# Kernel tuning notes

Measured on AMD Instinct MI355X. Metric: run time of the kernel, lower is better.

## Reference

```python
import jax, jax.numpy as jnp
import numpy as np

# dims: C=d_model, DI=expand*C (d_inner), S=d_state, R=dt_rank, K=4 scan dirs
C, DI, S, R, K = 64, 128, 16, 4, 4
Hh, Ww, T, Bsz = 48, 48, 4, 1

def _silu(x):
    return x * jax.nn.sigmoid(x)

def _ln_c(x, w, b, eps=1e-6):
    # LayerNorm2d: normalize over channel dim of [B,C,H,W]
    mu = jnp.mean(x, axis=1, keepdims=True)
    var = jnp.var(x, axis=1, keepdims=True)
    return (x - mu) * jax.lax.rsqrt(var + eps) * w[None, :, None, None] + b[None, :, None, None]

def _cal_kl(cur, prev):
    # elementwise KL over channel-softmax distributions, shape-preserving
    lp = jax.nn.log_softmax(prev, axis=1)
    lq = jax.nn.log_softmax(cur, axis=1)
    return jnp.exp(lp) * (lp - lq)

def _ss2d(x, in_w, in_b, cw, cb, xp_w, dt_w, dt_b, A_logs, Ds, onw, onb, ow, ob):
    # VMamba-style SS2D, channel-first input [B,C,H,W]
    B_, _, H_, W_ = x.shape
    L = H_ * W_
    xz = jnp.einsum('dc,bchw->bdhw', in_w, x) + in_b[None, :, None, None]
    xc, z = jnp.split(xz, 2, axis=1)
    di = xc.shape[1]
    xc = jax.lax.conv_general_dilated(xc, cw[:, None], (1, 1), 'SAME',
        dimension_numbers=('NCHW', 'OIHW', 'NCHW'), feature_group_count=di)
    xc = _silu(xc + cb[None, :, None, None])
    # cross-scan: row-major, col-major, and their reverses -> [B,K,DI,L]
    x1 = xc.reshape(B_, di, L)
    x2 = jnp.swapaxes(xc, 2, 3).reshape(B_, di, L)
    xs = jnp.stack([x1, x2, jnp.flip(x1, -1), jnp.flip(x2, -1)], axis=1)
    xdbl = jnp.einsum('krd,bkdl->bkrl', xp_w, xs)
    dts, Bs, Cs = jnp.split(xdbl, [R, R + S], axis=2)  # [B,K,R,L],[B,K,S,L],[B,K,S,L]
    dt = jax.nn.softplus(jnp.einsum('kdr,bkrl->bkdl', dt_w, dts) + dt_b[None, :, :, None])
    A = -jnp.exp(A_logs)  # [K,DI,S]
    dA = jnp.exp(dt[..., None] * A[None, :, :, None, :])                    # [B,K,DI,L,S]
    dBx = (dt * xs)[..., None] * jnp.swapaxes(Bs, 2, 3)[:, :, None, :, :]   # [B,K,DI,L,S]
    def comb(e1, e2):
        a1, b1 = e1
        a2, b2 = e2
        return (a1 * a2, a2 * b1 + b2)
    _, hs = jax.lax.associative_scan(comb, (dA, dBx), axis=3)
    y = jnp.einsum('bkdls,bksl->bkdl', hs, Cs) + Ds[None, :, :, None] * xs
    # cross-merge back to row-major and sum
    y0 = y[:, 0]
    y1 = jnp.swapaxes(y[:, 1].reshape(B_, di, W_, H_), 2, 3).reshape(B_, di, L)
    y2 = jnp.flip(y[:, 2], -1)
    y3 = jnp.swapaxes(jnp.flip(y[:, 3], -1).reshape(B_, di, W_, H_), 2, 3).reshape(B_, di, L)
    yy = (y0 + y1 + y2 + y3).reshape(B_, di, H_, W_)
    yy = _ln_c(yy, onw, onb) * _silu(z)
    return jnp.einsum('cd,bdhw->bchw', ow, yy) + ob[None, :, None, None]

def setup_inputs():
    key = jax.random.key(0)
    ks = jax.random.split(key, 16)
    rn = lambda k, shp, s: jax.random.normal(k, shp, jnp.float32) * s
    return {
        'image_sequence': rn(ks[0], (Bsz, T, C, Hh, Ww), 1.0),
        'difficult_zone': rn(ks[1], (Bsz, C, Hh, Ww), 1.0),
        'sigma': rn(ks[2], (Bsz, C, Hh, Ww), 0.1),
        # params stacked over the 2 SS2D modules: [0]=mamba_sigma, [1]=mamba_bias
        'in_w': rn(ks[3], (2, 2 * DI, C), C ** -0.5),
        'in_b': rn(ks[4], (2, 2 * DI), 0.02),
        'conv_w': rn(ks[5], (2, DI, 3, 3), 1.0 / 3.0),
        'conv_b': rn(ks[6], (2, DI), 0.02),
        'xp_w': rn(ks[7], (2, K, R + 2 * S, DI), DI ** -0.5),
        'dt_w': rn(ks[8], (2, K, DI, R), R ** -0.5),
        'dt_b': rn(ks[9], (2, K, DI), 0.5),
        'A_logs': jnp.log(1.0 + jax.random.uniform(ks[10], (2, K, DI, S), jnp.float32)),
        'Ds': rn(ks[11], (2, K, DI), 0.5),
        'onw': jnp.ones((2, DI), jnp.float32),
        'onb': jnp.zeros((2, DI), jnp.float32),
        'ow': rn(ks[12], (2, C, DI), 0.02),
        'ob': jnp.zeros((2, C), jnp.float32),
        'niw': jnp.ones((C,), jnp.float32),
        'nib': jnp.zeros((C,), jnp.float32),
        'ndw': jnp.ones((C,), jnp.float32),
        'ndb': jnp.zeros((C,), jnp.float32),
    }

def reference(image_sequence, difficult_zone, sigma, in_w, in_b, conv_w, conv_b, xp_w, dt_w, dt_b, A_logs, Ds, onw, onb, ow, ob, niw, nib, ndw, ndb):
    prev = _ln_c(difficult_zone, ndw, ndb)
    cur = prev * jnp.exp(sigma)  # prev / exp(-sigma)
    for t in range(T):  # strictly sequential recurrence over `length` steps
        s = _ss2d(_cal_kl(cur, prev), in_w[0], in_b[0], conv_w[0], conv_b[0], xp_w[0],
                  dt_w[0], dt_b[0], A_logs[0], Ds[0], onw[0], onb[0], ow[0], ob[0])
        bias = _ss2d(_ln_c(image_sequence[:, t], niw, nib), in_w[1], in_b[1], conv_w[1], conv_b[1], xp_w[1],
                     dt_w[1], dt_b[1], A_logs[1], Ds[1], onw[1], onb[1], ow[1], ob[1])
        cur, prev = cur * jnp.exp(s) + bias, cur
    return cur
```

## Files before the change

kernel.cpp:

```cpp
#include <hip/hip_runtime.h>

#define DEV __device__ __forceinline__

constexpr int Cc = 64, DIc = 128, Sc = 16, Rc = 4, Kc = 4;
constexpr int Lc = 2304, Tc = 4;
constexpr int NCH = 144, CHL = 16;

constexpr int OFF_XCPRE = 0;
constexpr int OFF_Z     = 294912;
constexpr int OFF_XACT  = 589824;
constexpr int OFF_DTS   = 884736;
constexpr int OFF_BS    = 921600;
constexpr int OFF_CS    = 1069056;
constexpr int OFF_Y     = 1216512;
constexpr int OFF_SUMA  = 2396160;
constexpr int OFF_SUMB  = 3575808;
constexpr int OFF_H0    = 4755456;
constexpr int SLOTF     = 5935104;
constexpr int OFF_B1    = 5 * SLOTF;
constexpr int OFF_B2    = OFF_B1 + Lc * Cc;
constexpr int OFF_BIAS  = OFF_B2 + Lc * Cc;
constexpr int OFF_TW    = OFF_BIAS + Tc * Lc * Cc;
constexpr int TW_INW  = 0;
constexpr int TW_XPW  = 32768;
constexpr int TW_OW   = 69632;
constexpr int TW_CW   = 86016;
constexpr int TW_AT   = 88320;
constexpr int TW_DTW  = 104704;

struct Params {
  const float *img, *dz, *sigma, *in_w, *in_b, *conv_w, *conv_b, *xp_w, *dt_w,
              *dt_b, *A_logs, *Ds, *onw, *onb, *ow, *ob, *niw, *nib, *ndw, *ndb;
  float* outp;
  float* ws;
};

DEV float wsum(float v) {
#pragma unroll
  for (int m = 32; m; m >>= 1) v += __shfl_xor(v, m, 64);
  return v;
}
DEV float wmax(float v) {
#pragma unroll
  for (int m = 32; m; m >>= 1) v = fmaxf(v, __shfl_xor(v, m, 64));
  return v;
}
DEV float sigmoidf(float x) { return 1.f / (1.f + __expf(-x)); }
DEV float softplusf(float v) { return (v > 20.f) ? v : __logf(1.f + __expf(v)); }
DEV float fexp2(float x) { return __builtin_amdgcn_exp2f(x); }

DEV int perm_idx(int k, int l) {
  if (k == 0) return l;
  if (k == 1) return (l % 48) * 48 + l / 48;
  if (k == 2) return Lc - 1 - l;
  int pp = Lc - 1 - l;
  return (pp % 48) * 48 + pp / 48;
}

DEV int perm_stride(int k) {
  return (k == 0) ? 1 : (k == 1) ? 48 : (k == 2) ? -1 : -48;
}

__global__ __launch_bounds__(256) void g_transpose(Params p) {
  float* tw = p.ws + OFF_TW;
  int i = blockIdx.x * 256 + threadIdx.x;
  if (i < 32768) {
    int d = i & 255, cc = (i >> 8) & 63, b = i >> 14;
    tw[TW_INW + i] = p.in_w[(b * 256 + d) * 64 + cc];
  }
  if (i < 36864) {
    int kr = i % 144, cc = (i / 144) & 127, b = i / (144 * 128);
    tw[TW_XPW + i] = p.xp_w[(b * 144 + kr) * 128 + cc];
  }
  if (i < 16384) {
    int c = i & 63, d = (i >> 6) & 127, b = i >> 13;
    tw[TW_OW + i] = p.ow[(b * 64 + c) * 128 + d];
  }
  if (i < 2304) {
    int d = i & 127, kk = (i >> 7) % 9, b = i / 1152;
    tw[TW_CW + i] = p.conv_w[(b * 128 + d) * 9 + kk];
  }
  if (i < 16384) {
    int d = i & 127, bks = i >> 7;
    int s = bks & 15, bk = bks >> 4;
    tw[TW_AT + i] = -__expf(p.A_logs[(bk * 128 + d) * 16 + s]) * 1.4426950408889634f;
  }
  if (i < 4096) {
    int d = i & 127, bkr = i >> 7;
    int r = bkr & 3, bk = bkr >> 2;
    tw[TW_DTW + i] = p.dt_w[(bk * 128 + d) * 4 + r];
  }
}

__global__ __launch_bounds__(256) void g_inproj(Params p) {
  __shared__ float xv[8][64];
  int tid = threadIdx.x;
  int slot = blockIdx.y;
  int branch = (slot >= 4) ? 0 : 1;
  float* ws = p.ws;
  float* base = ws + (size_t)slot * SLOTF;
  float* xcpre = base + OFF_XCPRE;
  float* zbuf  = base + OFF_Z;
  const float* wT = ws + OFF_TW + TW_INW + branch * 64 * 256;
  int l0 = blockIdx.x * 8;
  int wv = tid >> 6, c = tid & 63;
#pragma unroll
  for (int q = 0; q < 2; q++) {
    int pp = wv * 2 + q;
    int l = l0 + pp;
    float x;
    if (branch == 1) {
      float v = p.img[(slot * Cc + c) * Lc + l];
      float mu = wsum(v) * (1.f / 64.f);
      float var = wsum(v * v) * (1.f / 64.f) - mu * mu;
      x = (v - mu) * rsqrtf(var + 1e-6f) * p.niw[c] + p.nib[c];
    } else {
      float v = p.dz[c * Lc + l];
      float mu = wsum(v) * (1.f / 64.f);
      float var = wsum(v * v) * (1.f / 64.f) - mu * mu;
      float pv = (v - mu) * rsqrtf(var + 1e-6f) * p.ndw[c] + p.ndb[c];
      float cv = pv * __expf(p.sigma[c * Lc + l]);
      (ws + OFF_B1)[l * Cc + c] = cv;
      float mp = wmax(pv);
      float sp = wsum(__expf(pv - mp));
      float lp = pv - mp - __logf(sp);
      float mq = wmax(cv);
      float sq = wsum(__expf(cv - mq));
      float lq = cv - mq - __logf(sq);
      x = __expf(lp) * (lp - lq);
    }
    xv[pp][c] = x;
  }
  __syncthreads();
  int d = tid;
  float acc[8];
#pragma unroll
  for (int q = 0; q < 8; q++) acc[q] = 0.f;
  for (int cc = 0; cc < Cc; cc++) {
    float wval = wT[cc * 256 + d];
#pragma unroll
    for (int q = 0; q < 8; q++) acc[q] += wval * xv[q][cc];
  }
  float bv = p.in_b[branch * 2 * DIc + d];
  if (d < DIc) {
#pragma unroll
    for (int q = 0; q < 8; q++) xcpre[(l0 + q) * DIc + d] = acc[q] + bv;
  } else {
    int dd = d - DIc;
#pragma unroll
    for (int q = 0; q < 8; q++) zbuf[(l0 + q) * DIc + dd] = acc[q] + bv;
  }
}

__global__ __launch_bounds__(256) void g_conv(Params p, int slot_base) {
  __shared__ float xv[4][DIc];
  int tid = threadIdx.x;
  int slot = slot_base + blockIdx.y;
  int branch = (slot >= 4) ? 0 : 1;
  float* ws = p.ws;
  float* base = ws + (size_t)slot * SLOTF;
  float* xcpre = base + OFF_XCPRE;
  float* xact  = base + OFF_XACT;
  float* dtsb  = base + OFF_DTS;
  float* Bsb   = base + OFF_BS;
  float* Csb   = base + OFF_CS;
  const float* cwT  = ws + OFF_TW + TW_CW + branch * 9 * 128;
  const float* xpwT = ws + OFF_TW + TW_XPW + branch * 128 * 144;
  int h = blockIdx.x / 12;
  int w0 = (blockIdx.x % 12) * 4;
  for (int it = tid; it < 4 * DIc; it += 256) {
    int d = it & (DIc - 1);
    int pp = it >> 7;
    int w = w0 + pp;
    float acc = 0.f;
#pragma unroll
    for (int kh = 0; kh < 3; kh++) {
      int hh = h + kh - 1;
      if ((unsigned)hh < 48u) {
#pragma unroll
        for (int kw = 0; kw < 3; kw++) {
          int wp = w + kw - 1;
          if ((unsigned)wp < 48u)
            acc += cwT[(kh * 3 + kw) * 128 + d] * xcpre[(hh * 48 + wp) * DIc + d];
        }
      }
    }
    float v = acc + p.conv_b[branch * DIc + d];
    float s = v * sigmoidf(v);
    xv[pp][d] = s;
    xact[(h * 48 + w) * DIc + d] = s;
  }
  __syncthreads();
  if (tid < Kc * 36) {
    int k = tid / 36, r = tid % 36;
    float acc[4] = {0.f, 0.f, 0.f, 0.f};
    for (int cc = 0; cc < DIc; cc++) {
      float wvv = xpwT[cc * 144 + tid];
#pragma unroll
      for (int pp = 0; pp < 4; pp++) acc[pp] += wvv * xv[pp][cc];
    }
#pragma unroll
    for (int pp = 0; pp < 4; pp++) {
      int w = w0 + pp;
      int lr = h * 48 + w, lcx = w * 48 + h;
      int pos = (k == 0) ? lr : (k == 1) ? lcx : (k == 2) ? (Lc - 1 - lr) : (Lc - 1 - lcx);
      if (r < Rc) dtsb[(k * Lc + pos) * Rc + r] = acc[pp];
      else if (r < Rc + Sc) Bsb[(k * Lc + pos) * Sc + (r - Rc)] = acc[pp];
      else Csb[(k * Lc + pos) * Sc + (r - Rc - Sc)] = acc[pp];
    }
  }
}

__global__ __launch_bounds__(256, 4) void g_scan1(Params p, int slot_base) {
  __shared__ alignas(16) float2 sDt[CHL][DIc];
  __shared__ alignas(16) float sB[CHL * Sc];
  __shared__ float sCT[2][DIc];
  int tid = threadIdx.x;
  int slot = slot_base + blockIdx.y;
  int branch = (slot >= 4) ? 0 : 1;
  float* ws = p.ws;
  float* base = ws + (size_t)slot * SLOTF;
  const float* xact = base + OFF_XACT;
  const float* Bsb  = base + OFF_BS;
  const float* dtsb = base + OFF_DTS;
  float* sumA = base + OFF_SUMA;
  float* sumB = base + OFF_SUMB;
  int bx = blockIdx.x;
  int k = bx / NCH, ch = bx - k * NCH;
  int d = tid & (DIc - 1);
  int sh = tid >> 7;
  int bk = branch * Kc + k;
  const float* AT   = ws + OFF_TW + TW_AT;
  const float* dtwT = ws + OFF_TW + TW_DTW;
  int l0 = ch * CHL;
  sB[tid] = Bsb[(k * Lc + l0) * Sc + tid];
  float A2[8];
#pragma unroll
  for (int j = 0; j < 8; j++) A2[j] = AT[(bk * 16 + sh * 8 + j) * 128 + d];
  int idx0 = perm_idx(k, l0);
  int st = perm_stride(k);
  float xw[8];
#pragma unroll
  for (int j = 0; j < 8; j++) xw[j] = xact[(idx0 + st * (sh * 8 + j)) * DIc + d];
  float4 dtq[8];
#pragma unroll
  for (int j = 0; j < 8; j++)
    dtq[j] = *(const float4*)(dtsb + (size_t)(k * Lc + l0 + sh * 8 + j) * 4);
  float dw0 = dtwT[(bk * 4 + 0) * 128 + d];
  float dw1 = dtwT[(bk * 4 + 1) * 128 + d];
  float dw2 = dtwT[(bk * 4 + 2) * 128 + d];
  float dw3 = dtwT[(bk * 4 + 3) * 128 + d];
  float db = p.dt_b[bk * DIc + d];
  float ct = 0.f;
#pragma unroll
  for (int j = 0; j < 8; j++) {
    float v = db + dw0 * dtq[j].x + dw1 * dtq[j].y + dw2 * dtq[j].z + dw3 * dtq[j].w;
    float dtv = softplusf(v);
    sDt[sh * 8 + j][d] = make_float2(dtv, dtv * xw[j]);
    ct += dtv;
  }
  sCT[sh][d] = ct;
  __syncthreads();
  float CT = sCT[0][d] + sCT[1][d];
  const float4* B4 = (const float4*)sB;
  float h0 = 0.f, h1 = 0.f, h2 = 0.f, h3 = 0.f, h4 = 0.f, h5 = 0.f, h6 = 0.f, h7 = 0.f;
#pragma unroll
  for (int ib = 0; ib < 4; ib++) {
    float2 dg[4];
    float4 Bg0[4], Bg1[4];
#pragma unroll
    for (int q = 0; q < 4; q++) {
      int i = ib * 4 + q;
      dg[q]  = sDt[i][d];
      Bg0[q] = B4[i * 4 + sh * 2];
      Bg1[q] = B4[i * 4 + sh * 2 + 1];
    }
#pragma unroll
    for (int q = 0; q < 4; q++) {
      float dtv = dg[q].x, dtx = dg[q].y;
#define STEP1(hh, bb, aa2) { float da = fexp2(dtv * (aa2)); hh = da * hh + dtx * (bb); }
      STEP1(h0, Bg0[q].x, A2[0]);
      STEP1(h1, Bg0[q].y, A2[1]);
      STEP1(h2, Bg0[q].z, A2[2]);
      STEP1(h3, Bg0[q].w, A2[3]);
      STEP1(h4, Bg1[q].x, A2[4]);
      STEP1(h5, Bg1[q].y, A2[5]);
      STEP1(h6, Bg1[q].z, A2[6]);
      STEP1(h7, Bg1[q].w, A2[7]);
#undef STEP1
    }
  }
  float* sa = sumA + ((size_t)(k * NCH + ch) * Sc + sh * 8) * DIc + d;
  float* sb = sumB + ((size_t)(k * NCH + ch) * Sc + sh * 8) * DIc + d;
#pragma unroll
  for (int j = 0; j < 8; j++) sa[j * DIc] = fexp2(A2[j] * CT);
  sb[0 * DIc] = h0; sb[1 * DIc] = h1; sb[2 * DIc] = h2; sb[3 * DIc] = h3;
  sb[4 * DIc] = h4; sb[5 * DIc] = h5; sb[6 * DIc] = h6; sb[7 * DIc] = h7;
}

__global__ __launch_bounds__(256) void g_mid(Params p, int slot_base) {
  int gid = blockIdx.x * 256 + threadIdx.x;
  int slot = slot_base + blockIdx.y;
  float* base = p.ws + (size_t)slot * SLOTF;
  const float* sumA = base + OFF_SUMA;
  const float* sumB = base + OFF_SUMB;
  float* h0 = base + OFF_H0;
  int d = gid & (DIc - 1);
  int s = (gid >> 7) & (Sc - 1);
  int k = gid >> 11;
  float h = 0.f;
  for (int g = 0; g < NCH / 16; g++) {
    float a[16], b[16];
#pragma unroll
    for (int j = 0; j < 16; j++) {
      int idx = ((k * NCH + g * 16 + j) * Sc + s) * DIc + d;
      a[j] = sumA[idx];
      b[j] = sumB[idx];
    }
#pragma unroll
    for (int j = 0; j < 16; j++) {
      int idx = ((k * NCH + g * 16 + j) * Sc + s) * DIc + d;
      h0[idx] = h;
      h = a[j] * h + b[j];
    }
  }
}

__global__ __launch_bounds__(256, 4) void g_scan2(Params p, int slot_base) {
  __shared__ alignas(16) float2 sDt[CHL][DIc];
  __shared__ alignas(16) float sB[CHL * Sc];
  __shared__ alignas(16) float sC[CHL * Sc];
  int tid = threadIdx.x;
  int slot = slot_base + blockIdx.y;
  int branch = (slot >= 4) ? 0 : 1;
  float* ws = p.ws;
  float* base = ws + (size_t)slot * SLOTF;
  const float* xact = base + OFF_XACT;
  const float* Bsb  = base + OFF_BS;
  const float* Csb  = base + OFF_CS;
  const float* dtsb = base + OFF_DTS;
  const float* h0b  = base + OFF_H0;
  float* yb = base + OFF_Y;
  int bx = blockIdx.x;
  int k = bx / NCH, ch = bx - k * NCH;
  int d = tid & (DIc - 1);
  int sh = tid >> 7;
  int bk = branch * Kc + k;
  const float* AT   = ws + OFF_TW + TW_AT;
  const float* dtwT = ws + OFF_TW + TW_DTW;
  int l0 = ch * CHL;
  sB[tid] = Bsb[(k * Lc + l0) * Sc + tid];
  sC[tid] = Csb[(k * Lc + l0) * Sc + tid];
  float A2[8];
#pragma unroll
  for (int j = 0; j < 8; j++) A2[j] = AT[(bk * 16 + sh * 8 + j) * 128 + d];
  float hr0, hr1, hr2, hr3, hr4, hr5, hr6, hr7;
  {
    const float* hp = h0b + ((size_t)(k * NCH + ch) * Sc + sh * 8) * DIc + d;
    hr0 = hp[0 * DIc]; hr1 = hp[1 * DIc]; hr2 = hp[2 * DIc]; hr3 = hp[3 * DIc];
    hr4 = hp[4 * DIc]; hr5 = hp[5 * DIc]; hr6 = hp[6 * DIc]; hr7 = hp[7 * DIc];
  }
  int idx0 = perm_idx(k, l0);
  int st = perm_stride(k);
  float xw[8];
#pragma unroll
  for (int j = 0; j < 8; j++) xw[j] = xact[(idx0 + st * (sh * 8 + j)) * DIc + d];
  float4 dtq[8];
#pragma unroll
  for (int j = 0; j < 8; j++)
    dtq[j] = *(const float4*)(dtsb + (size_t)(k * Lc + l0 + sh * 8 + j) * 4);
  float dw0 = dtwT[(bk * 4 + 0) * 128 + d];
  float dw1 = dtwT[(bk * 4 + 1) * 128 + d];
  float dw2 = dtwT[(bk * 4 + 2) * 128 + d];
  float dw3 = dtwT[(bk * 4 + 3) * 128 + d];
  float db = p.dt_b[bk * DIc + d];
  float Dv = p.Ds[bk * DIc + d];
#pragma unroll
  for (int j = 0; j < 8; j++) {
    float v = db + dw0 * dtq[j].x + dw1 * dtq[j].y + dw2 * dtq[j].z + dw3 * dtq[j].w;
    float dtv = softplusf(v);
    sDt[sh * 8 + j][d] = make_float2(dtv, dtv * xw[j]);
  }
  __syncthreads();
  const float4* B4 = (const float4*)sB;
  const float4* C4 = (const float4*)sC;
  float acc[CHL];
#pragma unroll
  for (int ib = 0; ib < 4; ib++) {
    float2 dg[4];
    float4 Bg0[4], Bg1[4];
#pragma unroll
    for (int q = 0; q < 4; q++) {
      int i = ib * 4 + q;
      dg[q]  = sDt[i][d];
      Bg0[q] = B4[i * 4 + sh * 2];
      Bg1[q] = B4[i * 4 + sh * 2 + 1];
    }
#pragma unroll
    for (int q = 0; q < 4; q++) {
      int i = ib * 4 + q;
      float4 Cg0 = C4[i * 4 + sh * 2];
      float4 Cg1 = C4[i * 4 + sh * 2 + 1];
      float dtv = dg[q].x, dtx = dg[q].y;
      float a = 0.f;
#define STEP(hh, bb, cc, aa2) { float da = fexp2(dtv * (aa2)); hh = da * hh + dtx * (bb); a += hh * (cc); }
      STEP(hr0, Bg0[q].x, Cg0.x, A2[0]);
      STEP(hr1, Bg0[q].y, Cg0.y, A2[1]);
      STEP(hr2, Bg0[q].z, Cg0.z, A2[2]);
      STEP(hr3, Bg0[q].w, Cg0.w, A2[3]);
      STEP(hr4, Bg1[q].x, Cg1.x, A2[4]);
      STEP(hr5, Bg1[q].y, Cg1.y, A2[5]);
      STEP(hr6, Bg1[q].z, Cg1.z, A2[6]);
      STEP(hr7, Bg1[q].w, Cg1.w, A2[7]);
#undef STEP
      acc[i] = a;
    }
  }
  if (sh == 0) {
#pragma unroll
    for (int j = 0; j < 8; j++) acc[j] += Dv * xw[j];
  } else {
#pragma unroll
    for (int j = 0; j < 8; j++) acc[8 + j] += Dv * xw[j];
  }
  __syncthreads();
  float* yred = (float*)sDt;
  if (sh == 1) {
#pragma unroll
    for (int i = 0; i < CHL; i++) yred[i * DIc + d] = acc[i];
  }
  __syncthreads();
  if (sh == 0) {
#pragma unroll
    for (int i = 0; i < CHL; i++)
      yb[(size_t)(k * Lc + l0 + i) * DIc + d] = acc[i] + yred[i * DIc + d];
  }
}

__global__ __launch_bounds__(256) void g_out_bias(Params p) {
  __shared__ float yy[4][DIc];
  __shared__ float ml[4][DIc];
  __shared__ float mnv[4], isv[4];
  int tid = threadIdx.x;
  int slot = blockIdx.y;
  float* ws = p.ws;
  float* base = ws + (size_t)slot * SLOTF;
  const float* yb = base + OFF_Y;
  const float* zb = base + OFF_Z;
  const float* owT = ws + OFF_TW + TW_OW + 128 * 64;
  float* biasb = ws + OFF_BIAS;
  int l0 = blockIdx.x * 4;
  for (int it = tid; it < 4 * DIc; it += 256) {
    int d = it & (DIc - 1), pp = it >> 7;
    int l = l0 + pp;
    int www = l % 48, hh = l / 48;
    int lr = l, lcx = www * 48 + hh;
    float v = yb[(0 * Lc + lr) * DIc + d] + yb[(1 * Lc + lcx) * DIc + d] +
              yb[(2 * Lc + (Lc - 1 - lr)) * DIc + d] +
              yb[(3 * Lc + (Lc - 1 - lcx)) * DIc + d];
    yy[pp][d] = v;
  }
  __syncthreads();
  {
    int wv = tid >> 6, c = tid & 63;
    float a = yy[wv][c], b = yy[wv][c + 64];
    float s1 = wsum(a + b);
    float s2 = wsum(a * a + b * b);
    float mu = s1 * (1.f / 128.f);
    float var = s2 * (1.f / 128.f) - mu * mu;
    if (c == 0) { mnv[wv] = mu; isv[wv] = rsqrtf(var + 1e-6f); }
  }
  __syncthreads();
  for (int it = tid; it < 4 * DIc; it += 256) {
    int d = it & (DIc - 1), pp = it >> 7;
    int l = l0 + pp;
    float m = (yy[pp][d] - mnv[pp]) * isv[pp] * p.onw[DIc + d] + p.onb[DIc + d];
    float zv = zb[l * DIc + d];
    ml[pp][d] = m * zv * sigmoidf(zv);
  }
  __syncthreads();
  {
    int pp = tid >> 6, c = tid & 63;
    int l = l0 + pp;
    float acc = p.ob[Cc + c];
    for (int d2 = 0; d2 < DIc; d2++) acc += owT[d2 * 64 + c] * ml[pp][d2];
    biasb[(slot * Lc + l) * Cc + c] = acc;
  }
}

__global__ __launch_bounds__(256) void g_out_s(Params p, int targ, int fuse, int finalw,
                                               const float* curb, float* nxtb) {
  __shared__ float yy[4][DIc];
  __shared__ float ml[4][DIc];
  __shared__ float xvs[4][64];
  __shared__ float mnv[4], isv[4];
  int tid = threadIdx.x;
  float* ws = p.ws;
  float* base = ws + (size_t)4 * SLOTF;
  const float* yb = base + OFF_Y;
  const float* zb = base + OFF_Z;
  float* xcpre = base + OFF_XCPRE;
  float* zbuf  = base + OFF_Z;
  const float* owT  = ws + OFF_TW + TW_OW;
  const float* inwT = ws + OFF_TW + TW_INW;
  const float* biasb = ws + OFF_BIAS;
  int l0 = blockIdx.x * 4;
  for (int it = tid; it < 4 * DIc; it += 256) {
    int d = it & (DIc - 1), pp = it >> 7;
    int l = l0 + pp;
    int www = l % 48, hh = l / 48;
    int lr = l, lcx = www * 48 + hh;
    float v = yb[(0 * Lc + lr) * DIc + d] + yb[(1 * Lc + lcx) * DIc + d] +
              yb[(2 * Lc + (Lc - 1 - lr)) * DIc + d] +
              yb[(3 * Lc + (Lc - 1 - lcx)) * DIc + d];
    yy[pp][d] = v;
  }
  __syncthreads();
  {
    int wv = tid >> 6, c = tid & 63;
    float a = yy[wv][c], b = yy[wv][c + 64];
    float s1 = wsum(a + b);
    float s2 = wsum(a * a + b * b);
    float mu = s1 * (1.f / 128.f);
    float var = s2 * (1.f / 128.f) - mu * mu;
    if (c == 0) { mnv[wv] = mu; isv[wv] = rsqrtf(var + 1e-6f); }
  }
  __syncthreads();
  for (int it = tid; it < 4 * DIc; it += 256) {
    int d = it & (DIc - 1), pp = it >> 7;
    int l = l0 + pp;
    float m = (yy[pp][d] - mnv[pp]) * isv[pp] * p.onw[d] + p.onb[d];
    float zv = zb[l * DIc + d];
    ml[pp][d] = m * zv * sigmoidf(zv);
  }
  __syncthreads();
  {
    int pp = tid >> 6, c = tid & 63;
    int l = l0 + pp;
    float acc = p.ob[c];
    for (int d2 = 0; d2 < DIc; d2++) acc += owT[d2 * 64 + c] * ml[pp][d2];
    float cv = curb[l * Cc + c];
    float nv = cv * __expf(acc) + biasb[(targ * Lc + l) * Cc + c];
    nxtb[l * Cc + c] = nv;
    if (finalw) p.outp[c * Lc + l] = nv;
    if (fuse) {
      float mp = wmax(cv);
      float sp = wsum(__expf(cv - mp));
      float lp = cv - mp - __logf(sp);
      float mq = wmax(nv);
      float sq = wsum(__expf(nv - mq));
      float lq = nv - mq - __logf(sq);
      xvs[pp][c] = __expf(lp) * (lp - lq);
    }
  }
  if (fuse) {
    __syncthreads();
    int d = tid;
    float acc[4] = {0.f, 0.f, 0.f, 0.f};
    for (int cc = 0; cc < Cc; cc++) {
      float wval = inwT[cc * 256 + d];
#pragma unroll
      for (int pp = 0; pp < 4; pp++) acc[pp] += wval * xvs[pp][cc];
    }
    float bv = p.in_b[d];
    if (d < DIc) {
#pragma unroll
      for (int pp = 0; pp < 4; pp++) xcpre[(l0 + pp) * DIc + d] = acc[pp] + bv;
    } else {
      int dd = d - DIc;
#pragma unroll
      for (int pp = 0; pp < 4; pp++) zbuf[(l0 + pp) * DIc + dd] = acc[pp] + bv;
    }
  }
}

extern "C" void kernel_launch(void* const* d_in, const int* in_sizes, int n_in,
                              void* d_out, int out_size, void* d_ws, size_t ws_size,
                              hipStream_t stream) {
  (void)in_sizes; (void)n_in; (void)out_size; (void)ws_size;
  Params p;
  p.img    = (const float*)d_in[0];
  p.dz     = (const float*)d_in[1];
  p.sigma  = (const float*)d_in[2];
  p.in_w   = (const float*)d_in[3];
  p.in_b   = (const float*)d_in[4];
  p.conv_w = (const float*)d_in[5];
  p.conv_b = (const float*)d_in[6];
  p.xp_w   = (const float*)d_in[7];
  p.dt_w   = (const float*)d_in[8];
  p.dt_b   = (const float*)d_in[9];
  p.A_logs = (const float*)d_in[10];
  p.Ds     = (const float*)d_in[11];
  p.onw    = (const float*)d_in[12];
  p.onb    = (const float*)d_in[13];
  p.ow     = (const float*)d_in[14];
  p.ob     = (const float*)d_in[15];
  p.niw    = (const float*)d_in[16];
  p.nib    = (const float*)d_in[17];
  p.ndw    = (const float*)d_in[18];
  p.ndb    = (const float*)d_in[19];
  p.outp   = (float*)d_out;
  p.ws     = (float*)d_ws;


  hipLaunchKernelGGL(g_transpose, dim3(144), dim3(256), 0, stream, p);
  hipLaunchKernelGGL(g_inproj, dim3(288, 5), dim3(256), 0, stream, p);
  hipLaunchKernelGGL(g_conv, dim3(576, 5), dim3(256), 0, stream, p, 0);
  hipLaunchKernelGGL(g_scan1, dim3(Kc * NCH, 5), dim3(256), 0, stream, p, 0);
  hipLaunchKernelGGL(g_mid, dim3(32, 5), dim3(256), 0, stream, p, 0);
  hipLaunchKernelGGL(g_scan2, dim3(Kc * NCH, 5), dim3(256), 0, stream, p, 0);
  hipLaunchKernelGGL(g_out_bias, dim3(576, 4), dim3(256), 0, stream, p);

  float* b1 = p.ws + OFF_B1;
  float* b2 = p.ws + OFF_B2;
  hipLaunchKernelGGL(g_out_s, dim3(576), dim3(256), 0, stream, p, 0, 1, 0,
                     (const float*)b1, b2);
  for (int t = 1; t < Tc; t++) {
    const float* curb = (t & 1) ? b2 : b1;
    float* nxtb       = (t & 1) ? b1 : b2;
    hipLaunchKernelGGL(g_conv, dim3(576, 1), dim3(256), 0, stream, p, 4);
    hipLaunchKernelGGL(g_scan1, dim3(Kc * NCH, 1), dim3(256), 0, stream, p, 4);
    hipLaunchKernelGGL(g_mid, dim3(32, 1), dim3(256), 0, stream, p, 4);
    hipLaunchKernelGGL(g_scan2, dim3(Kc * NCH, 1), dim3(256), 0, stream, p, 4);
    hipLaunchKernelGGL(g_out_s, dim3(576), dim3(256), 0, stream, p,
                       t, (t == Tc - 1) ? 0 : 1, (t == Tc - 1) ? 1 : 0, curb, nxtb);
  }
}
```

Measured before the change: 393.8 us.

## Store chunk dt-sums instead of decay products and pre-merge reversed scan pairs

scan1 now writes only the per-chunk cumulative dt (one value per channel) rather than 16 exp decay factors, and g_mid recomputes the decay with exp2 from A, cutting one large workspace write/read. scan2 is restructured into 512-thread blocks that process a forward direction and its reversed counterpart on the mirrored chunk together, summing their outputs in shared memory and writing the merged result in row-major order. The output kernels then read two buffers instead of gathering four permuted ones. This adds an extra barrier and larger blocks in scan2 and depends on correct mirrored index arithmetic.

```diff
diff --git a/kernel.cpp b/kernel.cpp
--- a/kernel.cpp
+++ b/kernel.cpp
@@ -13,7 +13,7 @@
 constexpr int OFF_BS    = 921600;
 constexpr int OFF_CS    = 1069056;
 constexpr int OFF_Y     = 1216512;
-constexpr int OFF_SUMA  = 2396160;
+constexpr int OFF_CT    = 2396160;
 constexpr int OFF_SUMB  = 3575808;
 constexpr int OFF_H0    = 4755456;
 constexpr int SLOTF     = 5935104;
@@ -223,7 +223,7 @@
   const float* xact = base + OFF_XACT;
   const float* Bsb  = base + OFF_BS;
   const float* dtsb = base + OFF_DTS;
-  float* sumA = base + OFF_SUMA;
+  float* ctb  = base + OFF_CT;
   float* sumB = base + OFF_SUMB;
   int bx = blockIdx.x;
   int k = bx / NCH, ch = bx - k * NCH;
@@ -290,10 +290,8 @@
 #undef STEP1
     }
   }
-  float* sa = sumA + ((size_t)(k * NCH + ch) * Sc + sh * 8) * DIc + d;
+  if (sh == 0) ctb[(size_t)(k * NCH + ch) * DIc + d] = CT;
   float* sb = sumB + ((size_t)(k * NCH + ch) * Sc + sh * 8) * DIc + d;
-#pragma unroll
-  for (int j = 0; j < 8; j++) sa[j * DIc] = fexp2(A2[j] * CT);
   sb[0 * DIc] = h0; sb[1 * DIc] = h1; sb[2 * DIc] = h2; sb[3 * DIc] = h3;
   sb[4 * DIc] = h4; sb[5 * DIc] = h5; sb[6 * DIc] = h6; sb[7 * DIc] = h7;
 }
@@ -301,35 +299,39 @@
 __global__ __launch_bounds__(256) void g_mid(Params p, int slot_base) {
   int gid = blockIdx.x * 256 + threadIdx.x;
   int slot = slot_base + blockIdx.y;
+  int branch = (slot >= 4) ? 0 : 1;
   float* base = p.ws + (size_t)slot * SLOTF;
-  const float* sumA = base + OFF_SUMA;
+  const float* ctb  = base + OFF_CT;
   const float* sumB = base + OFF_SUMB;
+  const float* AT   = p.ws + OFF_TW + TW_AT;
   float* h0 = base + OFF_H0;
   int d = gid & (DIc - 1);
   int s = (gid >> 7) & (Sc - 1);
   int k = gid >> 11;
+  int bk = branch * Kc + k;
+  float A2s = AT[(bk * 16 + s) * 128 + d];
   float h = 0.f;
   for (int g = 0; g < NCH / 16; g++) {
-    float a[16], b[16];
+    float ct[16], b[16];
 #pragma unroll
     for (int j = 0; j < 16; j++) {
-      int idx = ((k * NCH + g * 16 + j) * Sc + s) * DIc + d;
-      a[j] = sumA[idx];
-      b[j] = sumB[idx];
+      int chj = k * NCH + g * 16 + j;
+      ct[j] = ctb[(size_t)chj * DIc + d];
+      b[j]  = sumB[((size_t)chj * Sc + s) * DIc + d];
     }
 #pragma unroll
     for (int j = 0; j < 16; j++) {
       int idx = ((k * NCH + g * 16 + j) * Sc + s) * DIc + d;
       h0[idx] = h;
-      h = a[j] * h + b[j];
-    }
-  }
-}
-
-__global__ __launch_bounds__(256, 4) void g_scan2(Params p, int slot_base) {
-  __shared__ alignas(16) float2 sDt[CHL][DIc];
-  __shared__ alignas(16) float sB[CHL * Sc];
-  __shared__ alignas(16) float sC[CHL * Sc];
+      h = fexp2(A2s * ct[j]) * h + b[j];
+    }
+  }
+}
+
+__global__ __launch_bounds__(512, 4) void g_scan2(Params p, int slot_base) {
+  __shared__ alignas(16) float2 sDt[2][CHL][DIc];
+  __shared__ alignas(16) float sB[2][CHL * Sc];
+  __shared__ alignas(16) float sC[2][CHL * Sc];
   int tid = threadIdx.x;
   int slot = slot_base + blockIdx.y;
   int branch = (slot >= 4) ? 0 : 1;
@@ -340,17 +342,20 @@
   const float* Csb  = base + OFF_CS;
   const float* dtsb = base + OFF_DTS;
   const float* h0b  = base + OFF_H0;
-  float* yb = base + OFF_Y;
-  int bx = blockIdx.x;
-  int k = bx / NCH, ch = bx - k * NCH;
+  int pair = blockIdx.x / NCH, chA = blockIdx.x - pair * NCH;
   int d = tid & (DIc - 1);
-  int sh = tid >> 7;
+  int sh = (tid >> 7) & 1;
+  int dir = tid >> 8;
+  int k = pair + 2 * dir;
+  int ch = dir ? (NCH - 1 - chA) : chA;
   int bk = branch * Kc + k;
+  float* ypair = base + OFF_Y + (size_t)pair * Lc * DIc;
   const float* AT   = ws + OFF_TW + TW_AT;
   const float* dtwT = ws + OFF_TW + TW_DTW;
   int l0 = ch * CHL;
-  sB[tid] = Bsb[(k * Lc + l0) * Sc + tid];
-  sC[tid] = Csb[(k * Lc + l0) * Sc + tid];
+  int t8 = tid & 255;
+  sB[dir][t8] = Bsb[(k * Lc + l0) * Sc + t8];
+  sC[dir][t8] = Csb[(k * Lc + l0) * Sc + t8];
   float A2[8];
 #pragma unroll
   for (int j = 0; j < 8; j++) A2[j] = AT[(bk * 16 + sh * 8 + j) * 128 + d];
@@ -379,11 +384,11 @@
   for (int j = 0; j < 8; j++) {
     float v = db + dw0 * dtq[j].x + dw1 * dtq[j].y + dw2 * dtq[j].z + dw3 * dtq[j].w;
     float dtv = softplusf(v);
-    sDt[sh * 8 + j][d] = make_float2(dtv, dtv * xw[j]);
-  }
-  __syncthreads();
-  const float4* B4 = (const float4*)sB;
-  const float4* C4 = (const float4*)sC;
+    sDt[dir][sh * 8 + j][d] = make_float2(dtv, dtv * xw[j]);
+  }
+  __syncthreads();
+  const float4* B4 = (const float4*)sB[dir];
+  const float4* C4 = (const float4*)sC[dir];
   float acc[CHL];
 #pragma unroll
   for (int ib = 0; ib < 4; ib++) {
@@ -392,7 +397,7 @@
 #pragma unroll
     for (int q = 0; q < 4; q++) {
       int i = ib * 4 + q;
-      dg[q]  = sDt[i][d];
+      dg[q]  = sDt[dir][i][d];
       Bg0[q] = B4[i * 4 + sh * 2];
       Bg1[q] = B4[i * 4 + sh * 2 + 1];
     }
@@ -427,13 +432,19 @@
   float* yred = (float*)sDt;
   if (sh == 1) {
 #pragma unroll
-    for (int i = 0; i < CHL; i++) yred[i * DIc + d] = acc[i];
-  }
-  __syncthreads();
-  if (sh == 0) {
+    for (int i = 0; i < CHL; i++) yred[(dir * CHL + i) * DIc + d] = acc[i];
+  }
+  __syncthreads();
+  if (sh == 0 && dir == 1) {
+#pragma unroll
+    for (int i = 0; i < CHL; i++) yred[(CHL + i) * DIc + d] += acc[i];
+  }
+  __syncthreads();
+  if (sh == 0 && dir == 0) {
 #pragma unroll
     for (int i = 0; i < CHL; i++)
-      yb[(size_t)(k * Lc + l0 + i) * DIc + d] = acc[i] + yred[i * DIc + d];
+      ypair[(size_t)(idx0 + st * i) * DIc + d] =
+          acc[i] + yred[i * DIc + d] + yred[(CHL + (CHL - 1 - i)) * DIc + d];
   }
 }
 
@@ -445,20 +456,16 @@
   int slot = blockIdx.y;
   float* ws = p.ws;
   float* base = ws + (size_t)slot * SLOTF;
-  const float* yb = base + OFF_Y;
+  const float* y01 = base + OFF_Y;
+  const float* y23 = base + OFF_Y + Lc * DIc;
   const float* zb = base + OFF_Z;
   const float* owT = ws + OFF_TW + TW_OW + 128 * 64;
   float* biasb = ws + OFF_BIAS;
   int l0 = blockIdx.x * 4;
   for (int it = tid; it < 4 * DIc; it += 256) {
     int d = it & (DIc - 1), pp = it >> 7;
-    int l = l0 + pp;
-    int www = l % 48, hh = l / 48;
-    int lr = l, lcx = www * 48 + hh;
-    float v = yb[(0 * Lc + lr) * DIc + d] + yb[(1 * Lc + lcx) * DIc + d] +
-              yb[(2 * Lc + (Lc - 1 - lr)) * DIc + d] +
-              yb[(3 * Lc + (Lc - 1 - lcx)) * DIc + d];
-    yy[pp][d] = v;
+    size_t off = (size_t)(l0 + pp) * DIc + d;
+    yy[pp][d] = y01[off] + y23[off];
   }
   __syncthreads();
   {
@@ -497,7 +504,8 @@
   int tid = threadIdx.x;
   float* ws = p.ws;
   float* base = ws + (size_t)4 * SLOTF;
-  const float* yb = base + OFF_Y;
+  const float* y01 = base + OFF_Y;
+  const float* y23 = base + OFF_Y + Lc * DIc;
   const float* zb = base + OFF_Z;
   float* xcpre = base + OFF_XCPRE;
   float* zbuf  = base + OFF_Z;
@@ -507,13 +515,8 @@
   int l0 = blockIdx.x * 4;
   for (int it = tid; it < 4 * DIc; it += 256) {
     int d = it & (DIc - 1), pp = it >> 7;
-    int l = l0 + pp;
-    int www = l % 48, hh = l / 48;
-    int lr = l, lcx = www * 48 + hh;
-    float v = yb[(0 * Lc + lr) * DIc + d] + yb[(1 * Lc + lcx) * DIc + d] +
-              yb[(2 * Lc + (Lc - 1 - lr)) * DIc + d] +
-              yb[(3 * Lc + (Lc - 1 - lcx)) * DIc + d];
-    yy[pp][d] = v;
+    size_t off = (size_t)(l0 + pp) * DIc + d;
+    yy[pp][d] = y01[off] + y23[off];
   }
   __syncthreads();
   {
@@ -608,7 +611,7 @@
   hipLaunchKernelGGL(g_conv, dim3(576, 5), dim3(256), 0, stream, p, 0);
   hipLaunchKernelGGL(g_scan1, dim3(Kc * NCH, 5), dim3(256), 0, stream, p, 0);
   hipLaunchKernelGGL(g_mid, dim3(32, 5), dim3(256), 0, stream, p, 0);
-  hipLaunchKernelGGL(g_scan2, dim3(Kc * NCH, 5), dim3(256), 0, stream, p, 0);
+  hipLaunchKernelGGL(g_scan2, dim3(2 * NCH, 5), dim3(512), 0, stream, p, 0);
   hipLaunchKernelGGL(g_out_bias, dim3(576, 4), dim3(256), 0, stream, p);
 
   float* b1 = p.ws + OFF_B1;
@@ -621,7 +624,7 @@
     hipLaunchKernelGGL(g_conv, dim3(576, 1), dim3(256), 0, stream, p, 4);
     hipLaunchKernelGGL(g_scan1, dim3(Kc * NCH, 1), dim3(256), 0, stream, p, 4);
     hipLaunchKernelGGL(g_mid, dim3(32, 1), dim3(256), 0, stream, p, 4);
-    hipLaunchKernelGGL(g_scan2, dim3(Kc * NCH, 1), dim3(256), 0, stream, p, 4);
+    hipLaunchKernelGGL(g_scan2, dim3(2 * NCH, 1), dim3(512), 0, stream, p, 4);
     hipLaunchKernelGGL(g_out_s, dim3(576), dim3(256), 0, stream, p,
                        t, (t == Tc - 1) ? 0 : 1, (t == Tc - 1) ? 1 : 0, curb, nxtb);
   }
```

Result: slower. 462.6 us (+17.5%).
